# Kernel optimization log

Measured on AMD Instinct MI355X. Metric: run time of the kernel, lower is better.

Reference implementation:

```python
import jax, jax.numpy as jnp
import numpy as np

B = 8            # graphs per batch (batch_size)
NPG = 4096       # nodes per graph
EPG = 65536      # edges per graph (avg degree 16)
IN = 384
K1, K2, K3 = 2458, 1475, 738   # ceil(.6*4096), ceil(.6*2458), ceil(.5*1475)
EPS = 1e-5


def setup_inputs() -> dict:
    key = jax.random.key(0)
    ks = jax.random.split(key, 16)
    x = jax.random.normal(ks[0], (B * NPG, IN), jnp.float32)
    off = (jnp.arange(B, dtype=jnp.int32) * NPG)[:, None]
    src = jax.random.randint(ks[1], (B, EPG), 0, NPG, dtype=jnp.int32) + off
    dst = jax.random.randint(ks[2], (B, EPG), 0, NPG, dtype=jnp.int32) + off
    edge_index = jnp.stack([src.reshape(-1), dst.reshape(-1)])

    def lin(k, i, o):
        return jax.random.normal(k, (i, o), jnp.float32) / np.sqrt(i)

    return dict(
        x=x, edge_index=edge_index,
        W1=lin(ks[3], IN, 512), b1=jnp.zeros(512, jnp.float32),
        W2=lin(ks[4], 512, 512), b2=jnp.zeros(512, jnp.float32),
        W3=lin(ks[5], 512, 256), b3=jnp.zeros(256, jnp.float32),
        W4=lin(ks[6], 256, 192), b4=jnp.zeros(192, jnp.float32),
        g1=jnp.ones(512, jnp.float32), be1=jnp.zeros(512, jnp.float32),
        g2=jnp.ones(512, jnp.float32), be2=jnp.zeros(512, jnp.float32),
        g3=jnp.ones(256, jnp.float32), be3=jnp.zeros(256, jnp.float32),
        p1_wrel=lin(ks[7], 512, 1), p1_brel=jnp.zeros(1, jnp.float32), p1_wroot=lin(ks[8], 512, 1),
        p2_wrel=lin(ks[9], 512, 1), p2_brel=jnp.zeros(1, jnp.float32), p2_wroot=lin(ks[10], 512, 1),
        p3_wrel=lin(ks[11], 256, 1), p3_brel=jnp.zeros(1, jnp.float32), p3_wroot=lin(ks[12], 256, 1),
    )


def _gcn_conv(x, W, b, src, dst, em, n):
    # PyG GCNConv(add_self_loops=False): h = D^-1/2 A D^-1/2 (x W) + b
    h = x @ W
    deg = jax.ops.segment_sum(em, dst, num_segments=n)           # in-degree of valid edges
    dis = jnp.where(deg > 0, jax.lax.rsqrt(jnp.maximum(deg, 1e-12)), 0.0)
    norm = (dis[src] * dis[dst] * em)[:, None]
    return jax.ops.segment_sum(h[src] * norm, dst, num_segments=n) + b


def _bn(x, g, b):
    # BatchNorm(track_running_stats=False): always batch stats, biased var
    mu = jnp.mean(x, axis=0)
    var = jnp.mean(jnp.square(x - mu), axis=0)
    return (x - mu) * jax.lax.rsqrt(var + EPS) * g + b


def _sag_score(x, wrel, brel, wroot, src, dst, em, n):
    # SAGPooling's GNN = GraphConv: lin_rel(sum_j x_j) + lin_root(x)
    agg = jax.ops.segment_sum(x[src] * em[:, None], dst, num_segments=n)
    return (agg @ wrel + brel + x @ wroot)[:, 0]


def _sag_pool(x, score, src, dst, em, npg, k):
    # per-graph top-k on raw scores; kept features scaled by tanh(score)
    topv, topi = jax.lax.top_k(score.reshape(B, npg), k)
    perm = (topi + (jnp.arange(B, dtype=jnp.int32) * npg)[:, None]).reshape(-1)
    xn = x[perm] * jnp.tanh(topv.reshape(-1))[:, None]
    inv = jnp.full(B * npg, -1, jnp.int32).at[perm].set(
        jnp.arange(B * k, dtype=jnp.int32))
    ns, nd = inv[src], inv[dst]
    keep = (ns >= 0) & (nd >= 0)
    em = em * keep.astype(x.dtype)
    return xn, jnp.where(keep, ns, 0), jnp.where(keep, nd, 0), em


def reference(x, edge_index,
              W1, b1, W2, b2, W3, b3, W4, b4,
              g1, be1, g2, be2, g3, be3,
              p1_wrel, p1_brel, p1_wroot,
              p2_wrel, p2_brel, p2_wroot,
              p3_wrel, p3_brel, p3_wroot,
              batch_size=8):
    src, dst = edge_index[0], edge_index[1]
    em = jnp.ones(src.shape[0], x.dtype)

    h = jax.nn.relu(_bn(_gcn_conv(x, W1, b1, src, dst, em, B * NPG), g1, be1))
    s = _sag_score(h, p1_wrel, p1_brel, p1_wroot, src, dst, em, B * NPG)
    h, src, dst, em = _sag_pool(h, s, src, dst, em, NPG, K1)

    h = jax.nn.relu(_bn(_gcn_conv(h, W2, b2, src, dst, em, B * K1), g2, be2))
    s = _sag_score(h, p2_wrel, p2_brel, p2_wroot, src, dst, em, B * K1)
    h, src, dst, em = _sag_pool(h, s, src, dst, em, K1, K2)

    h = jax.nn.relu(_bn(_gcn_conv(h, W3, b3, src, dst, em, B * K2), g3, be3))
    s = _sag_score(h, p3_wrel, p3_brel, p3_wroot, src, dst, em, B * K2)
    h, src, dst, em = _sag_pool(h, s, src, dst, em, K2, K3)

    h = _gcn_conv(h, W4, b4, src, dst, em, B * K3)      # [B*K3, 192]
    hg = h.reshape(B, K3, 192)
    return jnp.mean(hg, axis=1) + jnp.max(hg, axis=1)   # global mean + max pool
```

## Files before the change

kernel.cpp:

```cpp
#include <hip/hip_runtime.h>
#include <cmath>

#define E_TOTAL 524288
#define NB 8

using f32x4 = __attribute__((ext_vector_type(4))) float;
using s16x8 = __attribute__((ext_vector_type(8))) short;
using s16x4 = __attribute__((ext_vector_type(4))) short;

static inline int cdiv(int a, int b) { return (a + b - 1) / b; }

__device__ inline unsigned short bf16_rn(float x) {
  unsigned u = __float_as_uint(x);
  return (unsigned short)((u + 0x7FFFu + ((u >> 16) & 1u)) >> 16);
}
__device__ inline void split3(float x, short& h, short& m, short& l) {
  unsigned short hb = bf16_rn(x);
  h = (short)hb;
  float hf = __uint_as_float(((unsigned)hb) << 16);
  float r1 = x - hf;
  unsigned short mb = bf16_rn(r1);
  m = (short)mb;
  float mf = __uint_as_float(((unsigned)mb) << 16);
  l = (short)bf16_rn(r1 - mf);
}

__device__ inline void async_copy16(const short* g, short* l) {
  __builtin_amdgcn_global_load_lds(
      (const __attribute__((address_space(1))) void*)(unsigned long long)(g),
      (__attribute__((address_space(3))) void*)(unsigned)(unsigned long long)(l),
      16, 0, 0);
}

__global__ void fill_i32(int* p, int v, int n) {
  int i = blockIdx.x * 256 + threadIdx.x;
  if (i < n) p[i] = v;
}

__global__ void split_w_t(const float* __restrict__ W, short* __restrict__ TH,
                          short* __restrict__ TM, short* __restrict__ TL, int K, int N) {
  int i = blockIdx.x * 256 + threadIdx.x;
  if (i >= K * N) return;
  int k = i / N, n = i % N;
  short h, m, l;
  split3(W[i], h, m, l);
  TH[(size_t)n * K + k] = h;
  TM[(size_t)n * K + k] = m;
  TL[(size_t)n * K + k] = l;
}

#define GBM 128
#define GBN 256
#define GBK 32
#define BUFS 36864
#define BOFF 12288

__global__ __launch_bounds__(512) void gemm_mfma(
    const short* __restrict__ AH, const short* __restrict__ AM, const short* __restrict__ AL,
    const short* __restrict__ BH, const short* __restrict__ BM, const short* __restrict__ BL,
    const float* __restrict__ bias, float* __restrict__ C,
    int M, int K, int N, int nblocks) {
  __shared__ __align__(16) short lds[2][BUFS];
  int nwg = gridDim.x;
  int orig = blockIdx.x;
  int q = nwg >> 3, r = nwg & 7;
  int xc = orig & 7, j8 = orig >> 3;
  int wg = (xc < r ? xc * (q + 1) : r * (q + 1) + (xc - r) * q) + j8;
  int bm = (wg / nblocks) * GBM;
  int bn = (wg % nblocks) * GBN;
  int tid = threadIdx.x;
  int wave = tid >> 6, lane = tid & 63;
  int wr = wave >> 2, wc = wave & 3;
  int l15 = lane & 15, l4 = lane >> 4;
  int pa = wave * 64 + lane;
  int ra = pa >> 2, ca = (pa & 3) ^ ((ra >> 1) & 3);
  int gar = bm + ra; gar = gar < M ? gar : 0;
  size_t gaoff = (size_t)gar * K + ca * 8;
  int adest = wave * 512;
  int pb0 = wave * 128 + lane, pb1 = pb0 + 64;
  int rb0 = pb0 >> 2, cb0 = (pb0 & 3) ^ ((rb0 >> 1) & 3);
  int rb1 = pb1 >> 2, cb1 = (pb1 & 3) ^ ((rb1 >> 1) & 3);
  int gbr0 = bn + rb0; gbr0 = gbr0 < N ? gbr0 : 0;
  int gbr1 = bn + rb1; gbr1 = gbr1 < N ? gbr1 : 0;
  size_t gboff0 = (size_t)gbr0 * K + cb0 * 8;
  size_t gboff1 = (size_t)gbr1 * K + cb1 * 8;
  int bdest = BOFF + wave * 1024;

  auto stage = [&](int b, int k0) {
    short* base = lds[b];
    async_copy16(AH + gaoff + k0, base + adest);
    async_copy16(AM + gaoff + k0, base + 4096 + adest);
    async_copy16(AL + gaoff + k0, base + 8192 + adest);
    async_copy16(BH + gboff0 + k0, base + bdest);
    async_copy16(BH + gboff1 + k0, base + bdest + 512);
    async_copy16(BM + gboff0 + k0, base + 8192 + bdest);
    async_copy16(BM + gboff1 + k0, base + 8192 + bdest + 512);
    async_copy16(BL + gboff0 + k0, base + 16384 + bdest);
    async_copy16(BL + gboff1 + k0, base + 16384 + bdest + 512);
  };

  f32x4 acc[4][4] = {};
  int cur = 0;
  stage(0, 0);
  __syncthreads();
  for (int k0 = 0; k0 < K; k0 += GBK) {
    if (k0 + GBK < K) stage(cur ^ 1, k0 + GBK);
    const short* base = lds[cur];
    s16x8 fah[4], fam[4], fal[4], fbh[4], fbm[4], fbl[4];
#pragma unroll
    for (int mi = 0; mi < 4; ++mi) {
      int row = wr * 64 + mi * 16 + l15;
      int ad = row * 32 + ((l4 ^ ((row >> 1) & 3)) << 3);
      fah[mi] = *(const s16x8*)(base + ad);
      fam[mi] = *(const s16x8*)(base + 4096 + ad);
      fal[mi] = *(const s16x8*)(base + 8192 + ad);
    }
#pragma unroll
    for (int ni = 0; ni < 4; ++ni) {
      int row = wc * 64 + ni * 16 + l15;
      int bd = BOFF + row * 32 + ((l4 ^ ((row >> 1) & 3)) << 3);
      fbh[ni] = *(const s16x8*)(base + bd);
      fbm[ni] = *(const s16x8*)(base + 8192 + bd);
      fbl[ni] = *(const s16x8*)(base + 16384 + bd);
    }
#pragma unroll
    for (int mi = 0; mi < 4; ++mi)
#pragma unroll
      for (int ni = 0; ni < 4; ++ni) {
        acc[mi][ni] = __builtin_amdgcn_mfma_f32_16x16x32_bf16(fah[mi], fbh[ni], acc[mi][ni], 0, 0, 0);
        acc[mi][ni] = __builtin_amdgcn_mfma_f32_16x16x32_bf16(fah[mi], fbm[ni], acc[mi][ni], 0, 0, 0);
        acc[mi][ni] = __builtin_amdgcn_mfma_f32_16x16x32_bf16(fam[mi], fbh[ni], acc[mi][ni], 0, 0, 0);
        acc[mi][ni] = __builtin_amdgcn_mfma_f32_16x16x32_bf16(fah[mi], fbl[ni], acc[mi][ni], 0, 0, 0);
        acc[mi][ni] = __builtin_amdgcn_mfma_f32_16x16x32_bf16(fal[mi], fbh[ni], acc[mi][ni], 0, 0, 0);
        acc[mi][ni] = __builtin_amdgcn_mfma_f32_16x16x32_bf16(fam[mi], fbm[ni], acc[mi][ni], 0, 0, 0);
      }
    __syncthreads();
    cur ^= 1;
  }
#pragma unroll
  for (int ni = 0; ni < 4; ++ni) {
    int col = bn + wc * 64 + ni * 16 + l15;
    if (col >= N) continue;
    float bv = bias ? bias[col] : 0.f;
#pragma unroll
    for (int mi = 0; mi < 4; ++mi) {
      int row0 = bm + wr * 64 + mi * 16 + l4 * 4;
#pragma unroll
      for (int rr = 0; rr < 4; ++rr) {
        int row = row0 + rr;
        if (row < M) C[(size_t)row * N + col] = acc[mi][ni][rr] + bv;
      }
    }
  }
}

__global__ void count_kernel(const int* __restrict__ dst, int* __restrict__ cnt, int E) {
  int e = blockIdx.x * 256 + threadIdx.x;
  if (e >= E) return;
  atomicAdd(&cnt[dst[e]], 1);
}

__global__ __launch_bounds__(1024) void scan_kernel(const int* __restrict__ cnt,
                                                    int* __restrict__ offs,
                                                    float* __restrict__ dis, int n) {
  __shared__ int tsum[1024];
  int tid = threadIdx.x;
  int chunk = (n + 1023) / 1024;
  int base = tid * chunk;
  int lsum = 0;
  for (int i = 0; i < chunk; ++i) {
    int idx = base + i;
    if (idx < n) lsum += cnt[idx];
  }
  tsum[tid] = lsum;
  __syncthreads();
  for (int off = 1; off < 1024; off <<= 1) {
    int add = (tid >= off) ? tsum[tid - off] : 0;
    __syncthreads();
    tsum[tid] += add;
    __syncthreads();
  }
  int run = (tid == 0) ? 0 : tsum[tid - 1];
  for (int i = 0; i < chunk; ++i) {
    int idx = base + i;
    if (idx < n) {
      offs[idx] = run;
      int c = cnt[idx];
      run += c;
      dis[idx] = (c > 0) ? (float)(1.0 / sqrt((double)c)) : 0.f;
    }
  }
  if (tid == 1023) offs[n] = run;
}

__global__ void scatter_kernel(const int* __restrict__ src, const int* __restrict__ dst,
                               const int* __restrict__ offs, int* __restrict__ tmpc,
                               int* __restrict__ esrc, int E) {
  int e = blockIdx.x * 256 + threadIdx.x;
  if (e >= E) return;
  int d = dst[e];
  if (d < 0) return;
  int pos = offs[d] + atomicAdd(&tmpc[d], 1);
  esrc[pos] = src[e];
}

__global__ void sort_buckets(const int* __restrict__ offs, int* __restrict__ esrc, int n) {
  int node = blockIdx.x * 256 + threadIdx.x;
  if (node >= n) return;
  int s0 = offs[node], s1 = offs[node + 1];
  for (int i = s0 + 1; i < s1; ++i) {
    int v = esrc[i];
    int j = i - 1;
    while (j >= s0 && esrc[j] > v) { esrc[j + 1] = esrc[j]; --j; }
    esrc[j + 1] = v;
  }
}

__global__ __launch_bounds__(256) void agg_kernel(
    const float* __restrict__ h, const int* __restrict__ offs,
    const int* __restrict__ esrc, const float* __restrict__ dis,
    const float* __restrict__ bias, float* __restrict__ outf,
    short* __restrict__ outh, short* __restrict__ outm, short* __restrict__ outl,
    int F, int n) {
  int node = blockIdx.x * 4 + (threadIdx.x >> 6);
  if (node >= n) return;
  int lane = threadIdx.x & 63;
  int nf4 = F >> 2;
  int i0 = lane, i1 = lane + 64;
  bool a0 = i0 < nf4, a1 = i1 < nf4;
  f32x4 acc0 = {}, acc1 = {};
  int e0 = offs[node], e1 = offs[node + 1];
  int e = e0;
  for (; e + 4 <= e1; e += 4) {
    int s0 = esrc[e], s1 = esrc[e + 1], s2 = esrc[e + 2], s3 = esrc[e + 3];
    float w0 = dis[s0], w1 = dis[s1], w2 = dis[s2], w3 = dis[s3];
    const f32x4* p0 = (const f32x4*)(h + (size_t)s0 * F);
    const f32x4* p1 = (const f32x4*)(h + (size_t)s1 * F);
    const f32x4* p2 = (const f32x4*)(h + (size_t)s2 * F);
    const f32x4* p3 = (const f32x4*)(h + (size_t)s3 * F);
    if (a0) {
      f32x4 v0 = p0[i0], v1 = p1[i0], v2 = p2[i0], v3 = p3[i0];
      acc0 += v0 * w0;
      acc0 += v1 * w1;
      acc0 += v2 * w2;
      acc0 += v3 * w3;
    }
    if (a1) {
      f32x4 v0 = p0[i1], v1 = p1[i1], v2 = p2[i1], v3 = p3[i1];
      acc1 += v0 * w0;
      acc1 += v1 * w1;
      acc1 += v2 * w2;
      acc1 += v3 * w3;
    }
  }
  for (; e < e1; ++e) {
    int s = esrc[e];
    float w = dis[s];
    const f32x4* hp = (const f32x4*)(h + (size_t)s * F);
    if (a0) acc0 += hp[i0] * w;
    if (a1) acc1 += hp[i1] * w;
  }
  float wd = dis[node];
  acc0 *= wd;
  acc1 *= wd;
  if (outf) {
    const f32x4* b4 = (const f32x4*)bias;
    f32x4* op = (f32x4*)(outf + (size_t)node * F);
    if (a0) op[i0] = acc0 + b4[i0];
    if (a1) op[i1] = acc1 + b4[i1];
  } else {
    short hh[4], mm[4], ll[4];
    if (a0) {
#pragma unroll
      for (int c = 0; c < 4; ++c) split3(acc0[c], hh[c], mm[c], ll[c]);
      *(s16x4*)&outh[(size_t)node * F + i0 * 4] = *(s16x4*)hh;
      *(s16x4*)&outm[(size_t)node * F + i0 * 4] = *(s16x4*)mm;
      *(s16x4*)&outl[(size_t)node * F + i0 * 4] = *(s16x4*)ll;
    }
    if (a1) {
#pragma unroll
      for (int c = 0; c < 4; ++c) split3(acc1[c], hh[c], mm[c], ll[c]);
      *(s16x4*)&outh[(size_t)node * F + i1 * 4] = *(s16x4*)hh;
      *(s16x4*)&outm[(size_t)node * F + i1 * 4] = *(s16x4*)mm;
      *(s16x4*)&outl[(size_t)node * F + i1 * 4] = *(s16x4*)ll;
    }
  }
}

#define BNY 512
__global__ void bn_stats_part(const float* __restrict__ x, double* __restrict__ psum,
                              double* __restrict__ psq, int n, int F) {
  int col = blockIdx.x * 256 + threadIdx.x;
  if (col >= F) return;
  double s = 0., q = 0.;
  for (int r = blockIdx.y; r < n; r += gridDim.y) {
    double v = (double)x[(size_t)r * F + col];
    s += v;
    q += v * v;
  }
  psum[blockIdx.y * F + col] = s;
  psq[blockIdx.y * F + col] = q;
}

__global__ __launch_bounds__(64) void bn_reduce(
    const double* __restrict__ psum, const double* __restrict__ psq,
    const float* __restrict__ g, const float* __restrict__ be,
    float* __restrict__ scf, float* __restrict__ shf,
    double* __restrict__ scd, double* __restrict__ shd, int n, int F) {
  int c = blockIdx.x;
  int lane = threadIdx.x;
  double s = 0., q = 0.;
  for (int p = lane; p < BNY; p += 64) {
    s += psum[p * F + c];
    q += psq[p * F + c];
  }
#pragma unroll
  for (int o = 1; o < 64; o <<= 1) {
    s += __shfl_xor(s, o, 64);
    q += __shfl_xor(q, o, 64);
  }
  if (lane == 0) {
    double inv_n = 1.0 / (double)n;
    double mu = s * inv_n;
    double var = q * inv_n - mu * mu;
    if (var < 0.) var = 0.;
    double istd = 1.0 / sqrt(var + 1e-5);
    double sc = istd * (double)g[c];
    double sh = (double)be[c] - mu * sc;
    scd[c] = sc;
    shd[c] = sh;
    scf[c] = (float)sc;
    shf[c] = (float)sh;
  }
}

__global__ __launch_bounds__(256) void score_dots(
    const float* __restrict__ hx,
    const double* __restrict__ scd, const double* __restrict__ shd,
    const float* __restrict__ wrel, const float* __restrict__ wroot,
    double* __restrict__ t, double* __restrict__ r, int F, int n) {
  int row = blockIdx.x * 4 + (threadIdx.x >> 6);
  if (row >= n) return;
  int lane = threadIdx.x & 63;
  int nf4 = F >> 2;
  const f32x4* hp = (const f32x4*)(hx + (size_t)row * F);
  double dr = 0., dq = 0.;
  for (int j = lane; j < nf4; j += 64) {
    f32x4 hv = hp[j];
#pragma unroll
    for (int c = 0; c < 4; ++c) {
      double vd = (double)hv[c] * scd[j * 4 + c] + shd[j * 4 + c];
      vd = vd > 0. ? vd : 0.;
      dr += vd * (double)wrel[j * 4 + c];
      dq += vd * (double)wroot[j * 4 + c];
    }
  }
#pragma unroll
  for (int o = 1; o < 64; o <<= 1) {
    dr += __shfl_xor(dr, o, 64);
    dq += __shfl_xor(dq, o, 64);
  }
  if (lane == 0) { t[row] = dr; r[row] = dq; }
}

__global__ void score_kernel(const int* __restrict__ offs, const int* __restrict__ esrc,
                             const double* __restrict__ t, const double* __restrict__ r,
                             const float* __restrict__ brel, double* __restrict__ s, int n) {
  int i = blockIdx.x * 256 + threadIdx.x;
  if (i >= n) return;
  double acc = 0.;
  int e0 = offs[i], e1 = offs[i + 1];
  for (int e = e0; e < e1; ++e) acc += t[esrc[e]];
  s[i] = acc + r[i] + (double)brel[0];
}

__global__ __launch_bounds__(1024) void topk_select(
    const double* __restrict__ s, int n_pg, int k,
    int* __restrict__ perm, float* __restrict__ tanhv, int* __restrict__ inv) {
  __shared__ unsigned hist[256];
  __shared__ unsigned long long sPfx;
  __shared__ int sRem;
  __shared__ unsigned wsum[16];
  __shared__ unsigned woff[4];
  int g = blockIdx.x;
  int tid = threadIdx.x;
  const double* sg = s + (size_t)g * n_pg;
  auto keyof = [&](int i) -> unsigned long long {
    unsigned long long u = (unsigned long long)__double_as_longlong(sg[i]);
    u = (u >> 63) ? ~u : (u | 0x8000000000000000ULL);
    return ((u >> 12) << 12) | (unsigned long long)(4095 - i);
  };
  unsigned long long prefix = 0;
  int rem = k;
  for (int shift = 56; shift >= 0; shift -= 8) {
    if (tid < 256) hist[tid] = 0;
    __syncthreads();
    unsigned long long himask = (shift == 56) ? 0ULL : (~0ULL << (shift + 8));
    for (int i = tid; i < n_pg; i += 1024) {
      unsigned long long kk = keyof(i);
      if ((kk & himask) == prefix) {
        unsigned b = (unsigned)((kk >> shift) & 255);
        atomicAdd(&hist[b], 1u);
      }
    }
    __syncthreads();
    unsigned a = 0, v = 0;
    int slane = 0, swid = 0;
    if (tid < 256) {
      int rrev = 255 - tid;
      a = hist[tid];
      v = a;
      slane = rrev & 63;
      swid = rrev >> 6;
      for (int o = 1; o < 64; o <<= 1) {
        unsigned u2 = __shfl_down(v, o, 64);
        if (slane >= o) v += u2;
      }
      if (slane == 63) woff[swid] = v;
    }
    __syncthreads();
    if (tid < 256) {
      unsigned base2 = 0;
      for (int wi = 0; wi < swid; ++wi) base2 += woff[wi];
      unsigned Sinc = base2 + v;
      unsigned Sexc = Sinc - a;
      if ((int)Sexc < rem && (int)Sinc >= rem) {
        sPfx = prefix | (((unsigned long long)tid) << shift);
        sRem = rem - (int)Sexc;
      }
    }
    __syncthreads();
    prefix = sPfx;
    rem = sRem;
    __syncthreads();
  }
  unsigned long long Kstar = prefix;
  int c = (n_pg + 1023) / 1024;
  int base = tid * c;
  int loc[4];
  int cnt = 0;
#pragma unroll 4
  for (int j = 0; j < c; ++j) {
    int i = base + j;
    int sel = (i < n_pg && keyof(i) >= Kstar) ? 1 : 0;
    loc[j] = cnt;
    cnt += sel;
  }
  int lane = tid & 63, wid = tid >> 6;
  int v2 = cnt;
  for (int o = 1; o < 64; o <<= 1) {
    int u2 = __shfl_up(v2, o, 64);
    if (lane >= o) v2 += u2;
  }
  int wexcl = v2 - cnt;
  if (lane == 63) wsum[wid] = (unsigned)v2;
  __syncthreads();
  if (tid == 0) {
    unsigned run = 0;
    for (int wi = 0; wi < 16; ++wi) { unsigned t2 = wsum[wi]; wsum[wi] = run; run += t2; }
  }
  __syncthreads();
  int offset = (int)wsum[wid] + wexcl;
  for (int j = 0; j < c; ++j) {
    int i = base + j;
    if (i >= n_pg) break;
    bool sel = keyof(i) >= Kstar;
    int old_g = g * n_pg + i;
    if (sel) {
      int new_g = g * k + offset + loc[j];
      perm[new_g] = old_g;
      tanhv[new_g] = (float)tanh(sg[i]);
      inv[old_g] = new_g;
    } else {
      inv[old_g] = -1;
    }
  }
}

__global__ __launch_bounds__(256) void gather_split(
    const float* __restrict__ h, const int* __restrict__ perm,
    const float* __restrict__ tanhv,
    const float* __restrict__ scf, const float* __restrict__ shf,
    short* __restrict__ gh, short* __restrict__ gm,
    short* __restrict__ gl, int F, int nk) {
  int i = blockIdx.x * 4 + (threadIdx.x >> 6);
  if (i >= nk) return;
  int lane = threadIdx.x & 63;
  int nf4 = F >> 2;
  int p = perm[i];
  float tv = tanhv[i];
  const f32x4* hp = (const f32x4*)(h + (size_t)p * F);
  const f32x4* sc = (const f32x4*)scf;
  const f32x4* sh = (const f32x4*)shf;
  for (int j = lane; j < nf4; j += 64) {
    f32x4 v = hp[j] * sc[j] + sh[j];
#pragma unroll
    for (int c = 0; c < 4; ++c) v[c] = fmaxf(v[c], 0.f);
    v *= tv;
    short hh[4], mm[4], ll[4];
#pragma unroll
    for (int c = 0; c < 4; ++c) split3(v[c], hh[c], mm[c], ll[c]);
    *(s16x4*)&gh[(size_t)i * F + j * 4] = *(s16x4*)hh;
    *(s16x4*)&gm[(size_t)i * F + j * 4] = *(s16x4*)mm;
    *(s16x4*)&gl[(size_t)i * F + j * 4] = *(s16x4*)ll;
  }
}

__global__ void remap_kernel(const int* __restrict__ src_in, const int* __restrict__ dst_in,
                             const int* __restrict__ inv, int* __restrict__ src_out,
                             int* __restrict__ dst_out, int* __restrict__ cnt, int E) {
  int e = blockIdx.x * 256 + threadIdx.x;
  if (e >= E) return;
  int d = dst_in[e];
  int ns = -1, nd = -1;
  if (d >= 0) { ns = inv[src_in[e]]; nd = inv[d]; }
  if (ns >= 0 && nd >= 0) {
    src_out[e] = ns;
    dst_out[e] = nd;
    atomicAdd(&cnt[nd], 1);
  } else {
    src_out[e] = 0;
    dst_out[e] = -1;
  }
}

#define PCH 16
__global__ void pool_partial(const float* __restrict__ h, float* __restrict__ part,
                             int k3, int F) {
  int g = blockIdx.x, c = blockIdx.y;
  int tid = threadIdx.x;
  int chunk = (k3 + PCH - 1) / PCH;
  int r0 = c * chunk, r1 = min(r0 + chunk, k3);
  const float* base = h + (size_t)g * k3 * F;
  float sm = 0.f, mx = -INFINITY;
  for (int r = r0; r < r1; ++r) {
    float v = base[(size_t)r * F + tid];
    sm += v;
    mx = fmaxf(mx, v);
  }
  float* pp = part + (size_t)(g * PCH + c) * 2 * F;
  pp[tid] = sm;
  pp[F + tid] = mx;
}
__global__ void pool_final(const float* __restrict__ part, float* __restrict__ out,
                           int k3, int F) {
  int g = blockIdx.x;
  int tid = threadIdx.x;
  float sm = 0.f, mx = -INFINITY;
  for (int c = 0; c < PCH; ++c) {
    const float* pp = part + (size_t)(g * PCH + c) * 2 * F;
    sm += pp[tid];
    mx = fmaxf(mx, pp[F + tid]);
  }
  out[g * F + tid] = sm / (float)k3 + mx;
}

extern "C" void kernel_launch(void* const* d_in, const int* in_sizes, int n_in,
                              void* d_out, int out_size, void* d_ws, size_t ws_size,
                              hipStream_t stream) {
  const float* x0 = (const float*)d_in[0];
  const int* eidx = (const int*)d_in[1];
  const float* W1 = (const float*)d_in[2];  const float* b1 = (const float*)d_in[3];
  const float* W2 = (const float*)d_in[4];  const float* b2 = (const float*)d_in[5];
  const float* W3 = (const float*)d_in[6];  const float* b3 = (const float*)d_in[7];
  const float* W4 = (const float*)d_in[8];  const float* b4 = (const float*)d_in[9];
  const float* g1 = (const float*)d_in[10]; const float* be1 = (const float*)d_in[11];
  const float* g2 = (const float*)d_in[12]; const float* be2 = (const float*)d_in[13];
  const float* g3 = (const float*)d_in[14]; const float* be3 = (const float*)d_in[15];
  const float* p1r = (const float*)d_in[16]; const float* p1b = (const float*)d_in[17];
  const float* p1o = (const float*)d_in[18];
  const float* p2r = (const float*)d_in[19]; const float* p2b = (const float*)d_in[20];
  const float* p2o = (const float*)d_in[21];
  const float* p3r = (const float*)d_in[22]; const float* p3b = (const float*)d_in[23];
  const float* p3o = (const float*)d_in[24];

  char* w = (char*)d_ws;
  size_t off = 0;
  auto alloc = [&](size_t bytes) -> void* {
    void* p = w + off;
    off = (off + bytes + 255) & ~(size_t)255;
    return p;
  };
  float* BUF0 = (float*)alloc(32768ull * 512 * 4);
  float* BUF1 = (float*)alloc(19664ull * 512 * 4);
  short* XH = (short*)alloc(32768ull * 384 * 2);
  short* XM = (short*)alloc(32768ull * 384 * 2);
  short* XL = (short*)alloc(32768ull * 384 * 2);
  short* WTH = (short*)alloc(638976ull * 2);
  short* WTM = (short*)alloc(638976ull * 2);
  short* WTL = (short*)alloc(638976ull * 2);
  int* czone = (int*)alloc(65537ull * 4);
  int* cnt = czone;
  int* tmpc = czone + 32769;
  int* offs = (int*)alloc(32769 * 4);
  float* dis = (float*)alloc(32768 * 4);
  double* tvec = (double*)alloc(32768 * 8);
  double* rvec = (double*)alloc(32768 * 8);
  double* svec = (double*)alloc(32768 * 8);
  int* inv = (int*)alloc(32768 * 4);
  int* perm = (int*)alloc(32768 * 4);
  float* tanhv = (float*)alloc(32768 * 4);
  int* e0s = (int*)alloc(E_TOTAL * 4);
  int* e0d = (int*)alloc(E_TOTAL * 4);
  int* e1s = (int*)alloc(E_TOTAL * 4);
  int* e1d = (int*)alloc(E_TOTAL * 4);
  int* esrc = (int*)alloc(E_TOTAL * 4);
  double* bnsum = (double*)alloc((size_t)BNY * 512 * 8);
  double* bnsq = (double*)alloc((size_t)BNY * 512 * 8);
  float* bnscf = (float*)alloc(512 * 4);
  float* bnshf = (float*)alloc(512 * 4);
  double* bnscd = (double*)alloc(512 * 8);
  double* bnshd = (double*)alloc(512 * 8);
  float* part = (float*)alloc((size_t)NB * PCH * 2 * 192 * 4);

  const int EB = cdiv(E_TOTAL, 256);

  auto build_csr = [&](const int* src, const int* dst, int n) {
    scan_kernel<<<1, 1024, 0, stream>>>(cnt, offs, dis, n);
    scatter_kernel<<<EB, 256, 0, stream>>>(src, dst, offs, tmpc, esrc, E_TOTAL);
    sort_buckets<<<cdiv(n, 256), 256, 0, stream>>>(offs, esrc, n);
  };

  auto pool = [&](float* hbuf, int n, int n_pg, int k, int F,
                  const float* g, const float* be, const float* wr, const float* wb,
                  const float* wo, const int* src, const int* dst, int* nsrc, int* ndst) {
    bn_stats_part<<<dim3(cdiv(F, 256), BNY), 256, 0, stream>>>(hbuf, bnsum, bnsq, n, F);
    bn_reduce<<<F, 64, 0, stream>>>(bnsum, bnsq, g, be, bnscf, bnshf, bnscd, bnshd, n, F);
    score_dots<<<cdiv(n, 4), 256, 0, stream>>>(hbuf, bnscd, bnshd, wr, wo, tvec, rvec, F, n);
    score_kernel<<<cdiv(n, 256), 256, 0, stream>>>(offs, esrc, tvec, rvec, wb, svec, n);
    topk_select<<<NB, 1024, 0, stream>>>(svec, n_pg, k, perm, tanhv, inv);
    gather_split<<<cdiv(NB * k, 4), 256, 0, stream>>>(hbuf, perm, tanhv, bnscf, bnshf, XH, XM, XL, F, NB * k);
    fill_i32<<<cdiv(65537, 256), 256, 0, stream>>>(czone, 0, 65537);
    remap_kernel<<<EB, 256, 0, stream>>>(src, dst, inv, nsrc, ndst, cnt, E_TOTAL);
  };

  split_w_t<<<cdiv(384 * 512, 256), 256, 0, stream>>>(W1, WTH, WTM, WTL, 384, 512);
  split_w_t<<<cdiv(512 * 512, 256), 256, 0, stream>>>(W2, WTH + 196608, WTM + 196608, WTL + 196608, 512, 512);
  split_w_t<<<cdiv(512 * 256, 256), 256, 0, stream>>>(W3, WTH + 458752, WTM + 458752, WTL + 458752, 512, 256);
  split_w_t<<<cdiv(256 * 192, 256), 256, 0, stream>>>(W4, WTH + 589824, WTM + 589824, WTL + 589824, 256, 192);

  fill_i32<<<cdiv(65537, 256), 256, 0, stream>>>(czone, 0, 65537);
  count_kernel<<<EB, 256, 0, stream>>>(eidx + E_TOTAL, cnt, E_TOTAL);
  build_csr(eidx, eidx + E_TOTAL, 32768);
  agg_kernel<<<cdiv(32768, 4), 256, 0, stream>>>(x0, offs, esrc, dis, nullptr, nullptr, XH, XM, XL, 384, 32768);
  gemm_mfma<<<cdiv(32768, 128) * 2, 512, 0, stream>>>(XH, XM, XL, WTH, WTM, WTL, b1, BUF0, 32768, 384, 512, 2);
  pool(BUF0, 32768, 4096, 2458, 512, g1, be1, p1r, p1b, p1o, eidx, eidx + E_TOTAL, e0s, e0d);

  build_csr(e0s, e0d, 19664);
  gemm_mfma<<<cdiv(19664, 128) * 2, 512, 0, stream>>>(XH, XM, XL, WTH + 196608, WTM + 196608, WTL + 196608, nullptr, BUF0, 19664, 512, 512, 2);
  agg_kernel<<<cdiv(19664, 4), 256, 0, stream>>>(BUF0, offs, esrc, dis, b2, BUF1, nullptr, nullptr, nullptr, 512, 19664);
  pool(BUF1, 19664, 2458, 1475, 512, g2, be2, p2r, p2b, p2o, e0s, e0d, e1s, e1d);

  build_csr(e1s, e1d, 11800);
  gemm_mfma<<<cdiv(11800, 128), 512, 0, stream>>>(XH, XM, XL, WTH + 458752, WTM + 458752, WTL + 458752, nullptr, BUF0, 11800, 512, 256, 1);
  agg_kernel<<<cdiv(11800, 4), 256, 0, stream>>>(BUF0, offs, esrc, dis, b3, BUF1, nullptr, nullptr, nullptr, 256, 11800);
  pool(BUF1, 11800, 1475, 738, 256, g3, be3, p3r, p3b, p3o, e1s, e1d, e0s, e0d);

  build_csr(e0s, e0d, 5904);
  gemm_mfma<<<cdiv(5904, 128), 512, 0, stream>>>(XH, XM, XL, WTH + 589824, WTM + 589824, WTL + 589824, nullptr, BUF0, 5904, 256, 192, 1);
  agg_kernel<<<cdiv(5904, 4), 256, 0, stream>>>(BUF0, offs, esrc, dis, b4, BUF1, nullptr, nullptr, nullptr, 192, 5904);
  pool_partial<<<dim3(NB, PCH), 192, 0, stream>>>(BUF1, part, 738, 192);
  pool_final<<<NB, 192, 0, stream>>>(part, (float*)d_out, 738, 192);
}
```

Measured before the change: 961.5 us.

## Fuse score aggregation into top-k kernel and relax GEMM double-buffer barriers

Removes the separate score_kernel and computes each graph's SAG scores directly inside topk_select, keeping them in a 4096-entry shared-memory array instead of a global score vector. This drops one launch and a global round-trip, and the radix passes now read LDS rather than global memory. The cost is that only 8 blocks now do the edge aggregation, so that work has far less parallelism. The GEMM loop also replaces __syncthreads with explicit vmcnt waits plus raw barriers, so the prefetch of the next tile stays in flight while the current tile is computed.

```diff
diff --git a/kernel.cpp b/kernel.cpp
--- a/kernel.cpp
+++ b/kernel.cpp
@@ -102,9 +102,17 @@
   f32x4 acc[4][4] = {};
   int cur = 0;
   stage(0, 0);
-  __syncthreads();
+  asm volatile("s_waitcnt vmcnt(0)" ::: "memory");
+  __builtin_amdgcn_s_barrier();
   for (int k0 = 0; k0 < K; k0 += GBK) {
-    if (k0 + GBK < K) stage(cur ^ 1, k0 + GBK);
+    if (k0 + GBK < K) {
+      stage(cur ^ 1, k0 + GBK);
+      asm volatile("s_waitcnt vmcnt(9)" ::: "memory");
+    } else {
+      asm volatile("s_waitcnt vmcnt(0)" ::: "memory");
+    }
+    __builtin_amdgcn_s_barrier();
+    __builtin_amdgcn_sched_barrier(0);
     const short* base = lds[cur];
     s16x8 fah[4], fam[4], fal[4], fbh[4], fbm[4], fbl[4];
 #pragma unroll
@@ -134,7 +142,7 @@
         acc[mi][ni] = __builtin_amdgcn_mfma_f32_16x16x32_bf16(fal[mi], fbh[ni], acc[mi][ni], 0, 0, 0);
         acc[mi][ni] = __builtin_amdgcn_mfma_f32_16x16x32_bf16(fam[mi], fbm[ni], acc[mi][ni], 0, 0, 0);
       }
-    __syncthreads();
+    __builtin_amdgcn_s_barrier();
     cur ^= 1;
   }
 #pragma unroll
@@ -363,20 +371,12 @@
   if (lane == 0) { t[row] = dr; r[row] = dq; }
 }
 
-__global__ void score_kernel(const int* __restrict__ offs, const int* __restrict__ esrc,
-                             const double* __restrict__ t, const double* __restrict__ r,
-                             const float* __restrict__ brel, double* __restrict__ s, int n) {
-  int i = blockIdx.x * 256 + threadIdx.x;
-  if (i >= n) return;
-  double acc = 0.;
-  int e0 = offs[i], e1 = offs[i + 1];
-  for (int e = e0; e < e1; ++e) acc += t[esrc[e]];
-  s[i] = acc + r[i] + (double)brel[0];
-}
-
 __global__ __launch_bounds__(1024) void topk_select(
-    const double* __restrict__ s, int n_pg, int k,
+    const int* __restrict__ offs, const int* __restrict__ esrc,
+    const double* __restrict__ t, const double* __restrict__ r,
+    const float* __restrict__ brel, int n_pg, int k,
     int* __restrict__ perm, float* __restrict__ tanhv, int* __restrict__ inv) {
+  __shared__ double sscore[4096];
   __shared__ unsigned hist[256];
   __shared__ unsigned long long sPfx;
   __shared__ int sRem;
@@ -384,9 +384,17 @@
   __shared__ unsigned woff[4];
   int g = blockIdx.x;
   int tid = threadIdx.x;
-  const double* sg = s + (size_t)g * n_pg;
+  double bb = (double)brel[0];
+  for (int i = tid; i < n_pg; i += 1024) {
+    int gi = g * n_pg + i;
+    double acc = 0.;
+    int e0 = offs[gi], e1 = offs[gi + 1];
+    for (int e = e0; e < e1; ++e) acc += t[esrc[e]];
+    sscore[i] = acc + r[gi] + bb;
+  }
+  __syncthreads();
   auto keyof = [&](int i) -> unsigned long long {
-    unsigned long long u = (unsigned long long)__double_as_longlong(sg[i]);
+    unsigned long long u = (unsigned long long)__double_as_longlong(sscore[i]);
     u = (u >> 63) ? ~u : (u | 0x8000000000000000ULL);
     return ((u >> 12) << 12) | (unsigned long long)(4095 - i);
   };
@@ -469,7 +477,7 @@
     if (sel) {
       int new_g = g * k + offset + loc[j];
       perm[new_g] = old_g;
-      tanhv[new_g] = (float)tanh(sg[i]);
+      tanhv[new_g] = (float)tanh(sscore[i]);
       inv[old_g] = new_g;
     } else {
       inv[old_g] = -1;
@@ -596,7 +604,6 @@
   float* dis = (float*)alloc(32768 * 4);
   double* tvec = (double*)alloc(32768 * 8);
   double* rvec = (double*)alloc(32768 * 8);
-  double* svec = (double*)alloc(32768 * 8);
   int* inv = (int*)alloc(32768 * 4);
   int* perm = (int*)alloc(32768 * 4);
   float* tanhv = (float*)alloc(32768 * 4);
@@ -627,8 +634,7 @@
     bn_stats_part<<<dim3(cdiv(F, 256), BNY), 256, 0, stream>>>(hbuf, bnsum, bnsq, n, F);
     bn_reduce<<<F, 64, 0, stream>>>(bnsum, bnsq, g, be, bnscf, bnshf, bnscd, bnshd, n, F);
     score_dots<<<cdiv(n, 4), 256, 0, stream>>>(hbuf, bnscd, bnshd, wr, wo, tvec, rvec, F, n);
-    score_kernel<<<cdiv(n, 256), 256, 0, stream>>>(offs, esrc, tvec, rvec, wb, svec, n);
-    topk_select<<<NB, 1024, 0, stream>>>(svec, n_pg, k, perm, tanhv, inv);
+    topk_select<<<NB, 1024, 0, stream>>>(offs, esrc, tvec, rvec, wb, n_pg, k, perm, tanhv, inv);
     gather_split<<<cdiv(NB * k, 4), 256, 0, stream>>>(hbuf, perm, tanhv, bnscf, bnshf, XH, XM, XL, F, NB * k);
     fill_i32<<<cdiv(65537, 256), 256, 0, stream>>>(czone, 0, 65537);
     remap_kernel<<<EB, 256, 0, stream>>>(src, dst, inv, nsrc, ndst, cnt, E_TOTAL);
```

After: 1.030 ms. 7.2% more time.
